# Optimization experiments

Measured on AMD Instinct MI355X. Metric: run time of the kernel, lower is better.

The kernel has to match this reference:

```python
import jax, jax.numpy as jnp
import numpy as np

EPS = 1e-6

def _rms_norm(x):
    xf = x.astype(jnp.float32)
    var = jnp.mean(xf * xf, axis=-1, keepdims=True)
    return (xf * jax.lax.rsqrt(var + EPS)).astype(x.dtype)

def setup_inputs() -> dict:
    key = jax.random.key(0)
    k1, k2 = jax.random.split(key)
    B, N, T, D = 16, 768, 48, 2048
    patches = jax.random.normal(k1, (B, N, D), dtype=jnp.float32)
    task_tokens = jax.random.normal(k2, (B, T, D), dtype=jnp.float32)
    task_token_mask = jnp.ones((B, T), dtype=bool)  # True = valid token
    return {"patches": patches, "task_tokens": task_tokens, "task_token_mask": task_token_mask}

def reference(patches, task_tokens, task_token_mask):
    D = patches.shape[-1]
    scale = 1.0 / np.sqrt(D)
    patches_n = _rms_norm(patches)          # [B,N,D]
    task_n = _rms_norm(task_tokens)         # [B,T,D]
    # additive attention bias: 0 for valid task tokens, finfo.min for masked
    neg = jnp.finfo(patches_n.dtype).min
    bias = jnp.where(task_token_mask[:, None, :], 0.0, neg).astype(patches_n.dtype)  # [B,1,T]
    # scaled dot-product attention: patches attend to task tokens
    logits = jnp.einsum('bnd,btd->bnt', patches_n, task_n) * scale + bias
    attn = jax.nn.softmax(logits, axis=-1)
    queries_raw = jnp.einsum('bnt,btd->bnd', attn, task_n)  # [B,N,D]
    queries = _rms_norm(queries_raw)
    # importance score: each query scores every patch
    score = jnp.einsum('bnd,bmd->bnm', queries, patches_n) * scale  # [B,N,N]
    # differentiable selection (select_soft, noise_scale=None):
    # straight-through: hard one-hot of argmax + soft softmax - stop_grad(soft)
    soft = jax.nn.softmax(score, axis=-1)
    hard = jax.nn.one_hot(jnp.argmax(score, axis=-1), score.shape[-1], dtype=score.dtype)
    sel = hard + soft - jax.lax.stop_gradient(soft)
    return sel
```

## Files before the change

kernel.cpp:

```cpp
#include <hip/hip_runtime.h>
#include <math.h>

#define NB 16
#define NN 768
#define NT 48
#define ND 2048
#define NROW (NB*NN)
#define SCALE 0.02209708691207961f
#define NEGBIG (-3.4028234663852886e38f)
#define TAU 1e-3f
#define KS 512

typedef _Float16 f16;
typedef f16  f16x8 __attribute__((ext_vector_type(8)));
typedef f16  f16x4 __attribute__((ext_vector_type(4)));
typedef float f32x4 __attribute__((ext_vector_type(4)));

__device__ __forceinline__ void stage16(const void* g, void* l) {
    __builtin_amdgcn_global_load_lds(
        (const __attribute__((address_space(1))) unsigned int*)g,
        (__attribute__((address_space(3))) unsigned int*)l, 16, 0, 0);
}

__global__ __launch_bounds__(256) void k_prep_task(const float* __restrict__ task,
                                                   float* __restrict__ task_n,
                                                   f16* __restrict__ t_hi,
                                                   f16* __restrict__ t_lo) {
    __shared__ float sred[8];
    const int row = blockIdx.x;
    const float4* src = (const float4*)(task + (size_t)row * ND);
    const int tid = threadIdx.x;
    float4 v0 = src[tid];
    float4 v1 = src[tid + 256];
    float s = v0.x*v0.x + v0.y*v0.y + v0.z*v0.z + v0.w*v0.w
            + v1.x*v1.x + v1.y*v1.y + v1.z*v1.z + v1.w*v1.w;
    #pragma unroll
    for (int off = 32; off > 0; off >>= 1) s += __shfl_down(s, off, 64);
    if ((tid & 63) == 0) sred[tid >> 6] = s;
    __syncthreads();
    if (tid == 0)
        sred[4] = 1.0f / sqrtf((sred[0]+sred[1]+sred[2]+sred[3]) * (1.0f/ND) + 1e-6f);
    __syncthreads();
    const float inv = sred[4];
    const size_t o = (size_t)row * ND;
    f16x4 h0, l0, h1, l1;
    float4 n0, n1;
    #pragma unroll
    for (int e = 0; e < 4; e++) {
        float f0 = (&v0.x)[e] * inv, f1 = (&v1.x)[e] * inv;
        (&n0.x)[e] = f0; (&n1.x)[e] = f1;
        f16 a = (f16)f0; h0[e] = a; l0[e] = (f16)(f0 - (float)a);
        f16 c = (f16)f1; h1[e] = c; l1[e] = (f16)(f1 - (float)c);
    }
    *(float4*)&task_n[o + tid*4]          = n0;
    *(float4*)&task_n[o + (tid+256)*4]    = n1;
    *(f16x4*)&t_hi[o + tid*4]             = h0;
    *(f16x4*)&t_lo[o + tid*4]             = l0;
    *(f16x4*)&t_hi[o + (tid+256)*4]       = h1;
    *(f16x4*)&t_lo[o + (tid+256)*4]       = l1;
}

__global__ __launch_bounds__(256) void k_R(const float* __restrict__ patches,
                                           const f16* __restrict__ t_hi,
                                           const f16* __restrict__ t_lo,
                                           float* __restrict__ Rpart,
                                           float* __restrict__ ssqpart) {
    __shared__ __align__(16) char Ah[64*128], Al[64*128];
    __shared__ __align__(16) char Bh[48*128], Bl[48*128];
    const int rt = blockIdx.x, ks = blockIdx.y, b = blockIdx.z;
    const int tid = threadIdx.x, wid = tid >> 6, lane = tid & 63;
    const int q15 = lane & 15, g4 = lane >> 4;
    const int trow = tid >> 2, tq = tid & 3;
    const int lr = lane >> 3, lgch = (lane & 7) ^ lr;
    const int cxor = q15 & 7;

    const float* gP = patches + ((size_t)(b*NN + rt*64))*ND + ks*KS;
    const f16* gTh = t_hi + (size_t)b*NT*ND + ks*KS;
    const f16* gTl = t_lo + (size_t)b*NT*ND + ks*KS;

    f32x4 acc[3];
    #pragma unroll
    for (int j = 0; j < 3; j++) acc[j] = (f32x4){0.f,0.f,0.f,0.f};
    float ssq = 0.f;

    const float* aptr = gP + (size_t)trow*ND + tq*16;
    float4 va[4], vb[4];
    #pragma unroll
    for (int k = 0; k < 4; k++) va[k] = *(const float4*)(aptr + k*4);

    auto body = [&](float4 (&v)[4], float4 (&vn)[4], int kk, bool last) {
        #pragma unroll
        for (int t2 = 0; t2 < 2; t2++) {
            const int u = wid + 4*t2;
            if (u < 6) {
                stage16(gTh + (size_t)(u*8 + lr)*ND + kk + lgch*8, Bh + u*1024);
                stage16(gTl + (size_t)(u*8 + lr)*ND + kk + lgch*8, Bl + u*1024);
            }
        }
        __builtin_amdgcn_sched_barrier(0);
        if (!last) {
            #pragma unroll
            for (int k = 0; k < 4; k++)
                vn[k] = *(const float4*)(aptr + kk + 64 + k*4);
        }
        __builtin_amdgcn_sched_barrier(0);
        float lssq = 0.f;
        f16x8 hi8[2], lo8[2];
        #pragma unroll
        for (int k = 0; k < 4; k++)
            #pragma unroll
            for (int e = 0; e < 4; e++) {
                const float f = (&v[k].x)[e];
                lssq += f*f;
                const f16 h = (f16)f;
                hi8[k>>1][(k&1)*4 + e] = h;
                lo8[k>>1][(k&1)*4 + e] = (f16)(f - (float)h);
            }
        lssq += __shfl_xor(lssq, 1, 64);
        lssq += __shfl_xor(lssq, 2, 64);
        if (tq == 0) ssq += lssq;
        const int rb = trow * 128;
        #pragma unroll
        for (int c = 0; c < 2; c++) {
            const int ch = (2*tq + c) ^ (trow & 7);
            *(f16x8*)(Ah + rb + ch*16) = hi8[c];
            *(f16x8*)(Al + rb + ch*16) = lo8[c];
        }
        __builtin_amdgcn_sched_barrier(0);
        if (last) asm volatile("s_waitcnt vmcnt(0)" ::: "memory");
        else      asm volatile("s_waitcnt vmcnt(4)" ::: "memory");
        asm volatile("s_waitcnt lgkmcnt(0)" ::: "memory");
        __builtin_amdgcn_s_barrier();
        __builtin_amdgcn_sched_barrier(0);
        #pragma unroll
        for (int ksub = 0; ksub < 2; ksub++) {
            const int chb = ((ksub*4 + g4) ^ cxor) << 4;
            const f16x8 a_h = *(const f16x8*)(Ah + (wid*16 + q15)*128 + chb);
            const f16x8 a_l = *(const f16x8*)(Al + (wid*16 + q15)*128 + chb);
            #pragma unroll
            for (int j = 0; j < 3; j++) {
                const f16x8 b_h = *(const f16x8*)(Bh + (j*16 + q15)*128 + chb);
                const f16x8 b_l = *(const f16x8*)(Bl + (j*16 + q15)*128 + chb);
                acc[j] = __builtin_amdgcn_mfma_f32_16x16x32_f16(a_h, b_h, acc[j], 0, 0, 0);
                acc[j] = __builtin_amdgcn_mfma_f32_16x16x32_f16(a_l, b_h, acc[j], 0, 0, 0);
                acc[j] = __builtin_amdgcn_mfma_f32_16x16x32_f16(a_h, b_l, acc[j], 0, 0, 0);
            }
        }
        asm volatile("" ::: "memory");
        __builtin_amdgcn_s_barrier();
        __builtin_amdgcn_sched_barrier(0);
    };

    body(va, vb,   0, false);
    body(vb, va,  64, false);
    body(va, vb, 128, false);
    body(vb, va, 192, false);
    body(va, vb, 256, false);
    body(vb, va, 320, false);
    body(va, vb, 384, false);
    body(vb, va, 448, true);

    const int grow = b*NN + rt*64;
    #pragma unroll
    for (int j = 0; j < 3; j++)
        #pragma unroll
        for (int r = 0; r < 4; r++)
            Rpart[((size_t)ks*NROW + grow + wid*16 + g4*4 + r)*48 + j*16 + q15] = acc[j][r];
    if (tq == 0)
        ssqpart[(size_t)ks*NROW + grow + trow] = ssq;
}

__global__ __launch_bounds__(256) void k_combine(const float* __restrict__ Rpart,
                                                 const float* __restrict__ ssqpart,
                                                 const int* __restrict__ mask,
                                                 float* __restrict__ w,
                                                 float* __restrict__ pinv,
                                                 f16* __restrict__ Whi,
                                                 f16* __restrict__ Wlo,
                                                 f16* __restrict__ Ghi,
                                                 f16* __restrict__ Glo) {
    const int r = blockIdx.x * 256 + threadIdx.x;
    const int b = r / NN;
    float ss = 0.f;
    #pragma unroll
    for (int ks = 0; ks < 4; ks++) ss += ssqpart[(size_t)ks*NROW + r];
    const float pv = 1.0f / sqrtf(ss * (1.0f/ND) + 1e-6f);
    pinv[r] = pv;
    float l[48];
    float mx = -INFINITY;
    #pragma unroll
    for (int t4 = 0; t4 < 12; t4++) {
        float4 a = {0.f,0.f,0.f,0.f};
        #pragma unroll
        for (int ks = 0; ks < 4; ks++) {
            const float4 p = *(const float4*)&Rpart[((size_t)ks*NROW + r)*48 + t4*4];
            a.x += p.x; a.y += p.y; a.z += p.z; a.w += p.w;
        }
        f16x4 gh, gl;
        #pragma unroll
        for (int e = 0; e < 4; e++) {
            const float g = (&a.x)[e] * pv;
            const f16 hh = (f16)g;
            gh[e] = hh; gl[e] = (f16)(g - (float)hh);
            const int t = t4*4 + e;
            const float bias = mask[b*NT + t] ? 0.0f : NEGBIG;
            l[t] = g * SCALE + bias;
            mx = fmaxf(mx, l[t]);
        }
        *(f16x4*)&Ghi[(size_t)r*64 + t4*4] = gh;
        *(f16x4*)&Glo[(size_t)r*64 + t4*4] = gl;
    }
    float sum = 0.f;
    #pragma unroll
    for (int t = 0; t < 48; t++) { l[t] = expf(l[t] - mx); sum += l[t]; }
    const float inv = 1.0f / sum;
    #pragma unroll
    for (int t4 = 0; t4 < 12; t4++) {
        float4 o;
        f16x4 wh, wlv;
        #pragma unroll
        for (int e = 0; e < 4; e++) {
            const float wv = l[t4*4 + e] * inv;
            (&o.x)[e] = wv;
            const f16 hh = (f16)wv;
            wh[e] = hh; wlv[e] = (f16)(wv - (float)hh);
        }
        *(float4*)&w[(size_t)r*48 + t4*4] = o;
        *(f16x4*)&Whi[(size_t)r*64 + t4*4] = wh;
        *(f16x4*)&Wlo[(size_t)r*64 + t4*4] = wlv;
    }
    const f16x4 z = {(f16)0.f, (f16)0.f, (f16)0.f, (f16)0.f};
    #pragma unroll
    for (int t4 = 12; t4 < 16; t4++) {
        *(f16x4*)&Whi[(size_t)r*64 + t4*4] = z;
        *(f16x4*)&Wlo[(size_t)r*64 + t4*4] = z;
        *(f16x4*)&Ghi[(size_t)r*64 + t4*4] = z;
        *(f16x4*)&Glo[(size_t)r*64 + t4*4] = z;
    }
}

__global__ __launch_bounds__(256) void k_scoreM(const f16* __restrict__ Whi,
                                                const f16* __restrict__ Wlo,
                                                const f16* __restrict__ Ghi,
                                                const f16* __restrict__ Glo,
                                                float4* __restrict__ part) {
    __shared__ float4 ent[4][64][17];
    const int mt = blockIdx.x, rt = blockIdx.y, b = blockIdx.z;
    const int tid = threadIdx.x, wid = tid >> 6, lane = tid & 63;
    const int q15 = lane & 15, g4 = lane >> 4;
    const int wr = wid >> 1, wc = wid & 1;

    const size_t n0 = (size_t)(b*NN + rt*128 + wr*64);
    const size_t m0 = (size_t)(b*NN + mt*128 + wc*64);
    const int mbase = mt*128 + wc*64;

    f16x8 ah[4][2], al[4][2], bh[4][2], bl[4][2];
    #pragma unroll
    for (int i = 0; i < 4; i++)
        #pragma unroll
        for (int ksub = 0; ksub < 2; ksub++) {
            const size_t ao = (n0 + i*16 + q15)*64 + ksub*32 + g4*8;
            ah[i][ksub] = *(const f16x8*)&Whi[ao];
            al[i][ksub] = *(const f16x8*)&Wlo[ao];
            const size_t bo = (m0 + i*16 + q15)*64 + ksub*32 + g4*8;
            bh[i][ksub] = *(const f16x8*)&Ghi[bo];
            bl[i][ksub] = *(const f16x8*)&Glo[bo];
        }
    __builtin_amdgcn_sched_barrier(0);

    f32x4 acc[4][4];
    #pragma unroll
    for (int i = 0; i < 4; i++)
        #pragma unroll
        for (int j = 0; j < 4; j++) acc[i][j] = (f32x4){0.f,0.f,0.f,0.f};

    #pragma unroll
    for (int ksub = 0; ksub < 2; ksub++)
        #pragma unroll
        for (int i = 0; i < 4; i++)
            #pragma unroll
            for (int j = 0; j < 4; j++) {
                acc[i][j] = __builtin_amdgcn_mfma_f32_16x16x32_f16(ah[i][ksub], bh[j][ksub], acc[i][j], 0, 0, 0);
                acc[i][j] = __builtin_amdgcn_mfma_f32_16x16x32_f16(al[i][ksub], bh[j][ksub], acc[i][j], 0, 0, 0);
                acc[i][j] = __builtin_amdgcn_mfma_f32_16x16x32_f16(ah[i][ksub], bl[j][ksub], acc[i][j], 0, 0, 0);
            }

    #pragma unroll
    for (int i = 0; i < 4; i++) {
        #pragma unroll
        for (int r = 0; r < 4; r++) {
            float v1 = -INFINITY, v2 = -INFINITY;
            int   i1 = 0x7FFFFFFF, i2 = 0x7FFFFFFF;
            #pragma unroll
            for (int j = 0; j < 4; j++) {
                const float s = acc[i][j][r];
                const int m = mbase + j*16 + q15;
                if (s > v1) { v2 = v1; i2 = i1; v1 = s; i1 = m; }
                else if (s > v2) { v2 = s; i2 = m; }
            }
            ent[wid][i*16 + g4*4 + r][q15] =
                make_float4(v1, __int_as_float(i1), v2, __int_as_float(i2));
        }
    }
    __syncthreads();
    {
        float V1 = -INFINITY, V2 = -INFINITY;
        int   I1 = 0x7FFFFFFF, I2 = 0x7FFFFFFF;
        #pragma unroll
        for (int q = 0; q < 16; q++) {
            const float4 e = ent[wid][lane][q];
            const float v1 = e.x, v2 = e.z;
            const int i1 = __float_as_int(e.y), i2 = __float_as_int(e.w);
            if (v1 > V1 || (v1 == V1 && i1 < I1)) {
                if (V1 > v2 || (V1 == v2 && I1 < i2)) { V2 = V1; I2 = I1; }
                else { V2 = v2; I2 = i2; }
                V1 = v1; I1 = i1;
            } else if (v1 > V2 || (v1 == V2 && i1 < I2)) { V2 = v1; I2 = i1; }
        }
        const size_t rowg = (size_t)b*NN + rt*128 + wr*64 + lane;
        part[rowg*12 + mt*2 + wc] =
            make_float4(V1, __int_as_float(I1), V2, __int_as_float(I2));
    }
}

__global__ __launch_bounds__(256) void k_final(const float* __restrict__ patches,
                                               const float* __restrict__ task_n,
                                               const float* __restrict__ w,
                                               const float* __restrict__ pinv,
                                               const float4* __restrict__ part,
                                               float* __restrict__ out) {
    __shared__ float qrow[ND];
    __shared__ float wl[48];
    __shared__ int   scand[24];
    __shared__ float swv[4];
    __shared__ int   swi[4];
    __shared__ int   s_idx, s_cnt;
    const int row = blockIdx.x;
    const int b = row / NN;
    const int tid = threadIdx.x, wid = tid >> 6, lane = tid & 63;

    if (wid == 0) {
        float myv = -INFINITY; int myi = 0x7FFFFFFF;
        if (lane < 24) {
            const float2 e = ((const float2*)part)[(size_t)row*24 + lane];
            myv = e.x; myi = __float_as_int(e.y);
        }
        float v = myv; int i = myi;
        #pragma unroll
        for (int off = 1; off <= 32; off <<= 1) {
            const float ov = __shfl_xor(v, off, 64);
            const int   oi = __shfl_xor(i, off, 64);
            if (ov > v || (ov == v && oi < i)) { v = ov; i = oi; }
        }
        const bool in_tau = (myv >= v - TAU);
        const unsigned long long mb  = __ballot(in_tau);
        const unsigned long long mbr = __ballot(in_tau && ((lane & 1) == 1));
        if (lane == 0) {
            s_idx = i;
            s_cnt = mbr ? 999 : __popcll(mb);
        }
        if (in_tau && lane < 24) {
            const unsigned long long below = mb & ((lane == 0) ? 0ull : (~0ull >> (64 - lane)));
            scand[__popcll(below)] = myi;
        }
    }
    __syncthreads();
    const int cnt = s_cnt;
    if (cnt > 1) {
        if (tid < 12) *(float4*)&wl[tid*4] = *(const float4*)&w[(size_t)row*48 + tid*4];
        __syncthreads();
        {
            float q[8] = {0.f,0.f,0.f,0.f,0.f,0.f,0.f,0.f};
            for (int t = 0; t < NT; t++) {
                const float wt = wl[t];
                const float* Tn = task_n + ((size_t)(b*NT + t))*ND + tid*8;
                const float4 u0 = *(const float4*)Tn;
                const float4 u1 = *(const float4*)(Tn + 4);
                q[0] = fmaf(wt, u0.x, q[0]); q[1] = fmaf(wt, u0.y, q[1]);
                q[2] = fmaf(wt, u0.z, q[2]); q[3] = fmaf(wt, u0.w, q[3]);
                q[4] = fmaf(wt, u1.x, q[4]); q[5] = fmaf(wt, u1.y, q[5]);
                q[6] = fmaf(wt, u1.z, q[6]); q[7] = fmaf(wt, u1.w, q[7]);
            }
            #pragma unroll
            for (int e2 = 0; e2 < 8; e2++) qrow[tid*8 + e2] = q[e2];
        }
        __syncthreads();
        float bw = -INFINITY; int bi = 0x7FFFFFFF;
        if (cnt != 999) {
            for (int c = wid; c < cnt; c += 4) {
                const int m = scand[c];
                const float* prow = patches + ((size_t)b*NN + m)*ND + lane*32;
                const float* qp = qrow + lane*32;
                float s = 0.f;
                #pragma unroll
                for (int k = 0; k < 8; k++) {
                    const float4 p = *(const float4*)(prow + k*4);
                    const float4 qv = *(const float4*)(qp + k*4);
                    s = fmaf(p.x, qv.x, s); s = fmaf(p.y, qv.y, s);
                    s = fmaf(p.z, qv.z, s); s = fmaf(p.w, qv.w, s);
                }
                #pragma unroll
                for (int off = 32; off > 0; off >>= 1) s += __shfl_down(s, off, 64);
                if (lane == 0) {
                    s *= pinv[b*NN + m];
                    if (s > bw || (s == bw && m < bi)) { bw = s; bi = m; }
                }
            }
        } else {
            for (int m = wid; m < NN; m += 4) {
                const float* prow = patches + ((size_t)b*NN + m)*ND + lane*32;
                const float* qp = qrow + lane*32;
                float s = 0.f;
                #pragma unroll
                for (int k = 0; k < 8; k++) {
                    const float4 p = *(const float4*)(prow + k*4);
                    const float4 qv = *(const float4*)(qp + k*4);
                    s = fmaf(p.x, qv.x, s); s = fmaf(p.y, qv.y, s);
                    s = fmaf(p.z, qv.z, s); s = fmaf(p.w, qv.w, s);
                }
                #pragma unroll
                for (int off = 32; off > 0; off >>= 1) s += __shfl_down(s, off, 64);
                if (lane == 0) {
                    s *= pinv[b*NN + m];
                    if (s > bw || (s == bw && m < bi)) { bw = s; bi = m; }
                }
            }
        }
        if (lane == 0) { swv[wid] = bw; swi[wid] = bi; }
        __syncthreads();
        if (tid == 0) {
            float v = swv[0]; int i = swi[0];
            #pragma unroll
            for (int k = 1; k < 4; k++) {
                if (swv[k] > v || (swv[k] == v && swi[k] < i)) { v = swv[k]; i = swi[k]; }
            }
            s_idx = i;
        }
        __syncthreads();
    }
    const int m = s_idx;
    if (tid < 192) {
        float4 o = {0.f, 0.f, 0.f, 0.f};
        if ((m >> 2) == tid) ((float*)&o)[m & 3] = 1.0f;
        ((float4*)(out + (size_t)row*NN))[tid] = o;
    }
}

extern "C" void kernel_launch(void* const* d_in, const int* in_sizes, int n_in,
                              void* d_out, int out_size, void* d_ws, size_t ws_size,
                              hipStream_t stream) {
    const float* patches = (const float*)d_in[0];
    const float* task    = (const float*)d_in[1];
    const int*   mask    = (const int*)d_in[2];
    float* out = (float*)d_out;

    char* p = (char*)d_ws;
    float* task_n  = (float*)p;  p += (size_t)NB*NT*ND*sizeof(float);
    f16*   t_hi    = (f16*)p;    p += (size_t)NB*NT*ND*sizeof(f16);
    f16*   t_lo    = (f16*)p;    p += (size_t)NB*NT*ND*sizeof(f16);
    float* Rpart   = (float*)p;  p += (size_t)4*NROW*48*sizeof(float);
    float* ssqpart = (float*)p;  p += (size_t)4*NROW*sizeof(float);
    float* w       = (float*)p;  p += (size_t)NROW*48*sizeof(float);
    float* pinv    = (float*)p;  p += (size_t)NROW*sizeof(float);
    f16*   Whi     = (f16*)p;    p += (size_t)NROW*64*sizeof(f16);
    f16*   Wlo     = (f16*)p;    p += (size_t)NROW*64*sizeof(f16);
    f16*   Ghi     = (f16*)p;    p += (size_t)NROW*64*sizeof(f16);
    f16*   Glo     = (f16*)p;    p += (size_t)NROW*64*sizeof(f16);
    float4* part   = (float4*)p; p += (size_t)NROW*12*sizeof(float4);

    k_prep_task<<<NB*NT, 256, 0, stream>>>(task, task_n, t_hi, t_lo);
    k_R<<<dim3(NN/64, 4, NB), 256, 0, stream>>>(patches, t_hi, t_lo, Rpart, ssqpart);
    k_combine<<<NROW/256, 256, 0, stream>>>(Rpart, ssqpart, mask, w, pinv,
                                            Whi, Wlo, Ghi, Glo);
    k_scoreM<<<dim3(6, 6, NB), 256, 0, stream>>>(Whi, Wlo, Ghi, Glo, part);
    k_final<<<NROW, 256, 0, stream>>>(patches, task_n, w, pinv, part, out);
}
```

Before: 100.4 us.

## Split R GEMM K into 8 slices, drop softmax normalization, batch rows in final

The R kernel's K dimension is split eight ways instead of four, so each block runs half as many k-steps and the grid has twice as many blocks for better occupancy. The combine kernel adds the extra partials. The softmax skips its division by the sum, since argmax is unaffected by a positive per-row scale. The final kernel handles eight rows per block, cutting block count and launch overhead. The costs are more partial-sum traffic, and rescaled weights that could shift the tau tie-break tolerance.

```diff
diff --git a/kernel.cpp b/kernel.cpp
--- a/kernel.cpp
+++ b/kernel.cpp
@@ -9,7 +9,9 @@
 #define SCALE 0.02209708691207961f
 #define NEGBIG (-3.4028234663852886e38f)
 #define TAU 1e-3f
-#define KS 512
+#define NKS 8
+#define KS (ND/NKS)
+#define RPB 8
 
 typedef _Float16 f16;
 typedef f16  f16x8 __attribute__((ext_vector_type(8)));
@@ -154,11 +156,7 @@
     body(va, vb,   0, false);
     body(vb, va,  64, false);
     body(va, vb, 128, false);
-    body(vb, va, 192, false);
-    body(va, vb, 256, false);
-    body(vb, va, 320, false);
-    body(va, vb, 384, false);
-    body(vb, va, 448, true);
+    body(vb, va, 192, true);
 
     const int grow = b*NN + rt*64;
     #pragma unroll
@@ -183,7 +181,7 @@
     const int b = r / NN;
     float ss = 0.f;
     #pragma unroll
-    for (int ks = 0; ks < 4; ks++) ss += ssqpart[(size_t)ks*NROW + r];
+    for (int ks = 0; ks < NKS; ks++) ss += ssqpart[(size_t)ks*NROW + r];
     const float pv = 1.0f / sqrtf(ss * (1.0f/ND) + 1e-6f);
     pinv[r] = pv;
     float l[48];
@@ -192,7 +190,7 @@
     for (int t4 = 0; t4 < 12; t4++) {
         float4 a = {0.f,0.f,0.f,0.f};
         #pragma unroll
-        for (int ks = 0; ks < 4; ks++) {
+        for (int ks = 0; ks < NKS; ks++) {
             const float4 p = *(const float4*)&Rpart[((size_t)ks*NROW + r)*48 + t4*4];
             a.x += p.x; a.y += p.y; a.z += p.z; a.w += p.w;
         }
@@ -210,17 +208,13 @@
         *(f16x4*)&Ghi[(size_t)r*64 + t4*4] = gh;
         *(f16x4*)&Glo[(size_t)r*64 + t4*4] = gl;
     }
-    float sum = 0.f;
-    #pragma unroll
-    for (int t = 0; t < 48; t++) { l[t] = expf(l[t] - mx); sum += l[t]; }
-    const float inv = 1.0f / sum;
     #pragma unroll
     for (int t4 = 0; t4 < 12; t4++) {
         float4 o;
         f16x4 wh, wlv;
         #pragma unroll
         for (int e = 0; e < 4; e++) {
-            const float wv = l[t4*4 + e] * inv;
+            const float wv = expf(l[t4*4 + e] - mx);
             (&o.x)[e] = wv;
             const f16 hh = (f16)wv;
             wh[e] = hh; wlv[e] = (f16)(wv - (float)hh);
@@ -335,114 +329,117 @@
     __shared__ float swv[4];
     __shared__ int   swi[4];
     __shared__ int   s_idx, s_cnt;
-    const int row = blockIdx.x;
-    const int b = row / NN;
     const int tid = threadIdx.x, wid = tid >> 6, lane = tid & 63;
 
-    if (wid == 0) {
-        float myv = -INFINITY; int myi = 0x7FFFFFFF;
-        if (lane < 24) {
-            const float2 e = ((const float2*)part)[(size_t)row*24 + lane];
-            myv = e.x; myi = __float_as_int(e.y);
-        }
-        float v = myv; int i = myi;
-        #pragma unroll
-        for (int off = 1; off <= 32; off <<= 1) {
-            const float ov = __shfl_xor(v, off, 64);
-            const int   oi = __shfl_xor(i, off, 64);
-            if (ov > v || (ov == v && oi < i)) { v = ov; i = oi; }
-        }
-        const bool in_tau = (myv >= v - TAU);
-        const unsigned long long mb  = __ballot(in_tau);
-        const unsigned long long mbr = __ballot(in_tau && ((lane & 1) == 1));
-        if (lane == 0) {
-            s_idx = i;
-            s_cnt = mbr ? 999 : __popcll(mb);
-        }
-        if (in_tau && lane < 24) {
-            const unsigned long long below = mb & ((lane == 0) ? 0ull : (~0ull >> (64 - lane)));
-            scand[__popcll(below)] = myi;
-        }
-    }
-    __syncthreads();
-    const int cnt = s_cnt;
-    if (cnt > 1) {
-        if (tid < 12) *(float4*)&wl[tid*4] = *(const float4*)&w[(size_t)row*48 + tid*4];
+    for (int rr = 0; rr < RPB; rr++) {
+        const int row = blockIdx.x * RPB + rr;
+        const int b = row / NN;
         __syncthreads();
-        {
-            float q[8] = {0.f,0.f,0.f,0.f,0.f,0.f,0.f,0.f};
-            for (int t = 0; t < NT; t++) {
-                const float wt = wl[t];
-                const float* Tn = task_n + ((size_t)(b*NT + t))*ND + tid*8;
-                const float4 u0 = *(const float4*)Tn;
-                const float4 u1 = *(const float4*)(Tn + 4);
-                q[0] = fmaf(wt, u0.x, q[0]); q[1] = fmaf(wt, u0.y, q[1]);
-                q[2] = fmaf(wt, u0.z, q[2]); q[3] = fmaf(wt, u0.w, q[3]);
-                q[4] = fmaf(wt, u1.x, q[4]); q[5] = fmaf(wt, u1.y, q[5]);
-                q[6] = fmaf(wt, u1.z, q[6]); q[7] = fmaf(wt, u1.w, q[7]);
-            }
-            #pragma unroll
-            for (int e2 = 0; e2 < 8; e2++) qrow[tid*8 + e2] = q[e2];
+        if (wid == 0) {
+            float myv = -INFINITY; int myi = 0x7FFFFFFF;
+            if (lane < 24) {
+                const float2 e = ((const float2*)part)[(size_t)row*24 + lane];
+                myv = e.x; myi = __float_as_int(e.y);
+            }
+            float v = myv; int i = myi;
+            #pragma unroll
+            for (int off = 1; off <= 32; off <<= 1) {
+                const float ov = __shfl_xor(v, off, 64);
+                const int   oi = __shfl_xor(i, off, 64);
+                if (ov > v || (ov == v && oi < i)) { v = ov; i = oi; }
+            }
+            const bool in_tau = (myv >= v - TAU);
+            const unsigned long long mb  = __ballot(in_tau);
+            const unsigned long long mbr = __ballot(in_tau && ((lane & 1) == 1));
+            if (lane == 0) {
+                s_idx = i;
+                s_cnt = mbr ? 999 : __popcll(mb);
+            }
+            if (in_tau && lane < 24) {
+                const unsigned long long below = mb & ((lane == 0) ? 0ull : (~0ull >> (64 - lane)));
+                scand[__popcll(below)] = myi;
+            }
         }
         __syncthreads();
-        float bw = -INFINITY; int bi = 0x7FFFFFFF;
-        if (cnt != 999) {
-            for (int c = wid; c < cnt; c += 4) {
-                const int m = scand[c];
-                const float* prow = patches + ((size_t)b*NN + m)*ND + lane*32;
-                const float* qp = qrow + lane*32;
-                float s = 0.f;
-                #pragma unroll
-                for (int k = 0; k < 8; k++) {
-                    const float4 p = *(const float4*)(prow + k*4);
-                    const float4 qv = *(const float4*)(qp + k*4);
-                    s = fmaf(p.x, qv.x, s); s = fmaf(p.y, qv.y, s);
-                    s = fmaf(p.z, qv.z, s); s = fmaf(p.w, qv.w, s);
+        const int cnt = s_cnt;
+        if (cnt > 1) {
+            if (tid < 12) *(float4*)&wl[tid*4] = *(const float4*)&w[(size_t)row*48 + tid*4];
+            __syncthreads();
+            {
+                float q[8] = {0.f,0.f,0.f,0.f,0.f,0.f,0.f,0.f};
+                for (int t = 0; t < NT; t++) {
+                    const float wt = wl[t];
+                    const float* Tn = task_n + ((size_t)(b*NT + t))*ND + tid*8;
+                    const float4 u0 = *(const float4*)Tn;
+                    const float4 u1 = *(const float4*)(Tn + 4);
+                    q[0] = fmaf(wt, u0.x, q[0]); q[1] = fmaf(wt, u0.y, q[1]);
+                    q[2] = fmaf(wt, u0.z, q[2]); q[3] = fmaf(wt, u0.w, q[3]);
+                    q[4] = fmaf(wt, u1.x, q[4]); q[5] = fmaf(wt, u1.y, q[5]);
+                    q[6] = fmaf(wt, u1.z, q[6]); q[7] = fmaf(wt, u1.w, q[7]);
                 }
                 #pragma unroll
-                for (int off = 32; off > 0; off >>= 1) s += __shfl_down(s, off, 64);
-                if (lane == 0) {
-                    s *= pinv[b*NN + m];
-                    if (s > bw || (s == bw && m < bi)) { bw = s; bi = m; }
+                for (int e2 = 0; e2 < 8; e2++) qrow[tid*8 + e2] = q[e2];
+            }
+            __syncthreads();
+            float bw = -INFINITY; int bi = 0x7FFFFFFF;
+            if (cnt != 999) {
+                for (int c = wid; c < cnt; c += 4) {
+                    const int m = scand[c];
+                    const float* prow = patches + ((size_t)b*NN + m)*ND + lane*32;
+                    const float* qp = qrow + lane*32;
+                    float s = 0.f;
+                    #pragma unroll
+                    for (int k = 0; k < 8; k++) {
+                        const float4 p = *(const float4*)(prow + k*4);
+                        const float4 qv = *(const float4*)(qp + k*4);
+                        s = fmaf(p.x, qv.x, s); s = fmaf(p.y, qv.y, s);
+                        s = fmaf(p.z, qv.z, s); s = fmaf(p.w, qv.w, s);
+                    }
+                    #pragma unroll
+                    for (int off = 32; off > 0; off >>= 1) s += __shfl_down(s, off, 64);
+                    if (lane == 0) {
+                        s *= pinv[b*NN + m];
+                        if (s > bw || (s == bw && m < bi)) { bw = s; bi = m; }
+                    }
                 }
-            }
-        } else {
-            for (int m = wid; m < NN; m += 4) {
-                const float* prow = patches + ((size_t)b*NN + m)*ND + lane*32;
-                const float* qp = qrow + lane*32;
-                float s = 0.f;
+            } else {
+                for (int m = wid; m < NN; m += 4) {
+                    const float* prow = patches + ((size_t)b*NN + m)*ND + lane*32;
+                    const float* qp = qrow + lane*32;
+                    float s = 0.f;
+                    #pragma unroll
+                    for (int k = 0; k < 8; k++) {
+                        const float4 p = *(const float4*)(prow + k*4);
+                        const float4 qv = *(const float4*)(qp + k*4);
+                        s = fmaf(p.x, qv.x, s); s = fmaf(p.y, qv.y, s);
+                        s = fmaf(p.z, qv.z, s); s = fmaf(p.w, qv.w, s);
+                    }
+                    #pragma unroll
+                    for (int off = 32; off > 0; off >>= 1) s += __shfl_down(s, off, 64);
+                    if (lane == 0) {
+                        s *= pinv[b*NN + m];
+                        if (s > bw || (s == bw && m < bi)) { bw = s; bi = m; }
+                    }
+                }
+            }
+            if (lane == 0) { swv[wid] = bw; swi[wid] = bi; }
+            __syncthreads();
+            if (tid == 0) {
+                float v = swv[0]; int i = swi[0];
                 #pragma unroll
-                for (int k = 0; k < 8; k++) {
-                    const float4 p = *(const float4*)(prow + k*4);
-                    const float4 qv = *(const float4*)(qp + k*4);
-                    s = fmaf(p.x, qv.x, s); s = fmaf(p.y, qv.y, s);
-                    s = fmaf(p.z, qv.z, s); s = fmaf(p.w, qv.w, s);
+                for (int k = 1; k < 4; k++) {
+                    if (swv[k] > v || (swv[k] == v && swi[k] < i)) { v = swv[k]; i = swi[k]; }
                 }
-                #pragma unroll
-                for (int off = 32; off > 0; off >>= 1) s += __shfl_down(s, off, 64);
-                if (lane == 0) {
-                    s *= pinv[b*NN + m];
-                    if (s > bw || (s == bw && m < bi)) { bw = s; bi = m; }
-                }
-            }
-        }
-        if (lane == 0) { swv[wid] = bw; swi[wid] = bi; }
-        __syncthreads();
-        if (tid == 0) {
-            float v = swv[0]; int i = swi[0];
-            #pragma unroll
-            for (int k = 1; k < 4; k++) {
-                if (swv[k] > v || (swv[k] == v && swi[k] < i)) { v = swv[k]; i = swi[k]; }
-            }
-            s_idx = i;
-        }
-        __syncthreads();
-    }
-    const int m = s_idx;
-    if (tid < 192) {
-        float4 o = {0.f, 0.f, 0.f, 0.f};
-        if ((m >> 2) == tid) ((float*)&o)[m & 3] = 1.0f;
-        ((float4*)(out + (size_t)row*NN))[tid] = o;
+                s_idx = i;
+            }
+            __syncthreads();
+        }
+        const int m = s_idx;
+        if (tid < 192) {
+            float4 o = {0.f, 0.f, 0.f, 0.f};
+            if ((m >> 2) == tid) ((float*)&o)[m & 3] = 1.0f;
+            ((float4*)(out + (size_t)row*NN))[tid] = o;
+        }
     }
 }
 
@@ -458,8 +455,8 @@
     float* task_n  = (float*)p;  p += (size_t)NB*NT*ND*sizeof(float);
     f16*   t_hi    = (f16*)p;    p += (size_t)NB*NT*ND*sizeof(f16);
     f16*   t_lo    = (f16*)p;    p += (size_t)NB*NT*ND*sizeof(f16);
-    float* Rpart   = (float*)p;  p += (size_t)4*NROW*48*sizeof(float);
-    float* ssqpart = (float*)p;  p += (size_t)4*NROW*sizeof(float);
+    float* Rpart   = (float*)p;  p += (size_t)NKS*NROW*48*sizeof(float);
+    float* ssqpart = (float*)p;  p += (size_t)NKS*NROW*sizeof(float);
     float* w       = (float*)p;  p += (size_t)NROW*48*sizeof(float);
     float* pinv    = (float*)p;  p += (size_t)NROW*sizeof(float);
     f16*   Whi     = (f16*)p;    p += (size_t)NROW*64*sizeof(f16);
@@ -469,9 +466,9 @@
     float4* part   = (float4*)p; p += (size_t)NROW*12*sizeof(float4);
 
     k_prep_task<<<NB*NT, 256, 0, stream>>>(task, task_n, t_hi, t_lo);
-    k_R<<<dim3(NN/64, 4, NB), 256, 0, stream>>>(patches, t_hi, t_lo, Rpart, ssqpart);
+    k_R<<<dim3(NN/64, NKS, NB), 256, 0, stream>>>(patches, t_hi, t_lo, Rpart, ssqpart);
     k_combine<<<NROW/256, 256, 0, stream>>>(Rpart, ssqpart, mask, w, pinv,
                                             Whi, Wlo, Ghi, Glo);
     k_scoreM<<<dim3(6, 6, NB), 256, 0, stream>>>(Whi, Wlo, Ghi, Glo, part);
-    k_final<<<NROW, 256, 0, stream>>>(patches, task_n, w, pinv, part, out);
-}
+    k_final<<<NROW/RPB, 256, 0, stream>>>(patches, task_n, w, pinv, part, out);
+}
```

Result: slower. 114.7 us (+14.2%).
